# Kernel tuning notes

Measured on AMD Instinct MI355X. Metric: run time of the kernel, lower is better.

The kernel has to match this reference:

```python
import jax, jax.numpy as jnp
import numpy as np

B, N, F, K, FILT = 256, 256, 128, 4, 256  # batch mols, max_atom, Fin, Chebyshev order, nb_filter
EPS = float(np.spacing(np.float32(0)))    # matches np.spacing(0) in original degree normalization
D2_FLOOR = 1e-12                          # numerical floor for sqrt of pairwise sq-dist


def setup_inputs() -> dict:
    key = jax.random.key(0)
    ks = jax.random.split(key, 6)
    x = jax.random.normal(ks[0], (B, N, F), dtype=jnp.float32)
    lap_in = 0.1 * jax.random.normal(ks[1], (B, N, N), dtype=jnp.float32)  # input per-mol Laplacian
    n_atoms = jax.random.randint(ks[2], (B,), 64, N + 1, dtype=jnp.int32)  # ragged mol sizes
    r1 = float(np.sqrt(6.0 / (F + F)))
    M_L = jax.random.uniform(ks[3], (F, F), jnp.float32, -r1, r1)          # Mahalanobis metric
    r2 = float(np.sqrt(6.0 / (F * K + FILT)))
    weight = jax.random.uniform(ks[4], (F * K, FILT), jnp.float32, -r2, r2)
    bias = jnp.zeros((FILT,), jnp.float32)
    return {"x": x, "lap_in": lap_in, "n_atoms": n_atoms, "M_L": M_L, "weight": weight, "bias": bias}


def reference(x, lap_in, n_atoms, M_L, weight, bias):
    # mask[b,n] = 1 for real atoms, 0 for padding (replaces per-mol tf.slice + pad)
    mask = (jnp.arange(N)[None, :] < n_atoms[:, None]).astype(x.dtype)       # [B,N]
    x = x * mask[..., None]

    # ---- learned Laplacian: Mahalanobis RBF affinity + sym degree normalization ----
    xw = jnp.einsum('bnf,fg->bng', x, M_L)                                   # x @ M_L
    sq = jnp.sum(xw * xw, axis=-1)                                           # [B,N]
    d2 = sq[:, :, None] + sq[:, None, :] - 2.0 * jnp.einsum('bif,bjf->bij', xw, xw)
    eye = jnp.eye(N, dtype=x.dtype)
    off = mask[:, :, None] * mask[:, None, :] * (1.0 - eye)                  # valid off-diag pairs
    d2_safe = jnp.where(off > 0, jnp.maximum(d2, D2_FLOOR), 1.0)
    W = jnp.exp(-jnp.sqrt(d2_safe)) * off                                    # W[i,j]=exp(-dist), diag 0
    deg = jnp.sum(W, axis=1) + EPS                                           # W symmetric: axis0==axis1
    dinv = jnp.where(mask > 0, 1.0 / jnp.sqrt(deg), 0.0)                     # D^{-1/2} (0 on padding)
    # L = I - D^{-1/2} W D^{-1/2} (intended math of the original py_func)
    L_learn = eye[None] * mask[:, :, None] - dinv[:, :, None] * W * dinv[:, None, :]
    L = L_learn + lap_in * (mask[:, :, None] * mask[:, None, :])             # L + sliced input LL

    # ---- Chebyshev recurrence: x0=x, x1=Lx, xk = 2 L x_{k-1} - x_{k-2} ----
    x0 = x
    x1 = jnp.einsum('bij,bjf->bif', L, x0)
    xs = [x0, x1]
    for _ in range(2, K):
        x2 = 2.0 * jnp.einsum('bij,bjf->bif', L, x1) - x0
        xs.append(x2)
        x0, x1 = x1, x2
    # stack -> [B,N,F,K] then flatten (f,k) row-major, matching reshape([K,M,F])->transpose([1,2,0])->reshape([M,K*F])
    xc = jnp.stack(xs, axis=-1).reshape(B, N, F * K)

    out = jnp.einsum('bnd,do->bno', xc, weight) + bias                       # [B,N,FILT]
    out = jax.nn.relu(out * mask[..., None])                                 # pad-to-max_atom + relu
    return out, L_learn
```

## Files before the change

kernel.cpp:

```cpp
#include <hip/hip_runtime.h>
#include <math.h>

typedef __bf16 bf16;
typedef __bf16 bf16x8 __attribute__((ext_vector_type(8)));
typedef __bf16 bf16x4 __attribute__((ext_vector_type(4)));
typedef float f32x4 __attribute__((ext_vector_type(4)));

constexpr int cB = 256, cN = 256, cF = 128, cO = 256;
constexpr int BN = cB * cN;
constexpr float D2_FLOOR = 1e-12f;
constexpr float EPS_F = 1.401298464324817e-45f;

constexpr size_t OFF_XC  = 0;
constexpr size_t OFF_XW  = OFF_XC + (size_t)BN * 512 * 2;
constexpr size_t OFF_X0T = OFF_XW + (size_t)BN * 128 * 2;
constexpr size_t OFF_X1T = OFF_X0T + (size_t)cB * cF * cN * 2;
constexpr size_t OFF_X2T = OFF_X1T + (size_t)cB * cF * cN * 2;
constexpr size_t OFF_LB  = OFF_X2T + (size_t)cB * cF * cN * 2;
constexpr size_t OFF_WT  = OFF_LB + (size_t)cB * cN * cN * 2;
constexpr size_t OFF_MT  = OFF_WT + 512 * 256 * 2;
constexpr size_t OFF_SQ  = OFF_MT + 128 * 128 * 2;

__device__ __forceinline__ bf16x8 gfrag(const bf16* __restrict__ p, int ld,
                                        int lane, int k0) {
  return *(const bf16x8*)(p + (size_t)(lane & 15) * ld + k0 + 8 * (lane >> 4));
}

__device__ __forceinline__ f32x4 mfma(bf16x8 a, bf16x8 b, f32x4 c) {
  return __builtin_amdgcn_mfma_f32_16x16x32_bf16(a, b, c, 0, 0, 0);
}

__global__ __launch_bounds__(256) void k_prep(const float* __restrict__ x,
                                              const int* __restrict__ na_p,
                                              bf16* __restrict__ xc,
                                              bf16* __restrict__ x0T) {
  __shared__ __align__(16) bf16 T[64][132];
  int b = blockIdx.x >> 2, i0 = (blockIdx.x & 3) * 64;
  int tid = threadIdx.x;
  int na = na_p[b];
#pragma unroll
  for (int it = 0; it < 8; ++it) {
    int ir = it * 8 + (tid >> 5);
    int f0 = (tid & 31) * 4;
    int i = i0 + ir;
    float m = (i < na) ? 1.f : 0.f;
    float4 v = *(const float4*)(x + ((size_t)b * cN + i) * cF + f0);
    bf16x4 pk = {(bf16)(v.x * m), (bf16)(v.y * m), (bf16)(v.z * m), (bf16)(v.w * m)};
    *(bf16x4*)(xc + ((size_t)b * cN + i) * 512 + f0) = pk;
    *(bf16x4*)(&T[ir][f0]) = pk;
  }
  __syncthreads();
  int f = tid >> 1, half = tid & 1;
  bf16* od = x0T + ((size_t)b * cF + f) * cN + i0 + half * 32;
#pragma unroll
  for (int c = 0; c < 32; c += 4) {
    int ii = half * 32 + c;
    bf16x4 pk = {T[ii][f], T[ii + 1][f], T[ii + 2][f], T[ii + 3][f]};
    *(bf16x4*)(od + c) = pk;
  }
}

__global__ __launch_bounds__(256) void k_wt(const float* __restrict__ wgt,
                                            const float* __restrict__ ML,
                                            bf16* __restrict__ Wt,
                                            bf16* __restrict__ MT) {
  int id = blockIdx.x * 256 + threadIdx.x;
  if (id < 512 * 256) {
    int o = id >> 9, d = id & 511;
    int k = d >> 7, f = d & 127;
    Wt[id] = (bf16)wgt[(f * 4 + k) * 256 + o];
  } else {
    int id2 = id - 512 * 256;
    if (id2 < 128 * 128) {
      int g = id2 >> 7, f = id2 & 127;
      MT[id2] = (bf16)ML[f * 128 + g];
    }
  }
}

__global__ __launch_bounds__(256, 2) void k_xw2(const bf16* __restrict__ xc,
                                                const bf16* __restrict__ MT,
                                                bf16* __restrict__ xw,
                                                float* __restrict__ sq) {
  __shared__ float sqb[128];
  int tid = threadIdx.x, wid = tid >> 6, lane = tid & 63;
  int r0 = blockIdx.x * 128;
  const bf16* A = xc + (size_t)r0 * 512;
  const bf16* Bg = MT + (size_t)(wid * 32) * 128;
  f32x4 acc[8][2] = {};
#pragma unroll
  for (int ks = 0; ks < 4; ++ks) {
    int k0 = ks * 32;
    bf16x8 b0 = gfrag(Bg, 128, lane, k0);
    bf16x8 b1 = gfrag(Bg + 16 * 128, 128, lane, k0);
#pragma unroll
    for (int mf = 0; mf < 8; ++mf) {
      bf16x8 a = gfrag(A + (size_t)mf * 16 * 512, 512, lane, k0);
      acc[mf][0] = mfma(a, b0, acc[mf][0]);
      acc[mf][1] = mfma(a, b1, acc[mf][1]);
    }
  }
  if (tid < 128) sqb[tid] = 0.f;
  __syncthreads();
  int hi = lane >> 4, il = lane & 15;
#pragma unroll
  for (int mf = 0; mf < 8; ++mf) {
#pragma unroll
    for (int r = 0; r < 4; ++r) {
      int row = r0 + mf * 16 + 4 * hi + r;
      float s = 0.f;
#pragma unroll
      for (int nf = 0; nf < 2; ++nf) {
        bf16 v = (bf16)acc[mf][nf][r];
        xw[(size_t)row * cF + wid * 32 + nf * 16 + il] = v;
        float f = (float)v;
        s = fmaf(f, f, s);
      }
      s += __shfl_xor(s, 1); s += __shfl_xor(s, 2);
      s += __shfl_xor(s, 4); s += __shfl_xor(s, 8);
      if (il == 0) atomicAdd(&sqb[mf * 16 + 4 * hi + r], s);
    }
  }
  __syncthreads();
  if (tid < 128) sq[r0 + tid] = sqb[tid];
}

__global__ __launch_bounds__(512, 2) void k_gramL(const bf16* __restrict__ xw,
                                                  const float* __restrict__ sq,
                                                  const float* __restrict__ lap,
                                                  const int* __restrict__ na_p,
                                                  bf16* __restrict__ Lb,
                                                  float* __restrict__ llearn) {
  __shared__ float lsq[256];
  __shared__ float deg[256];
  __shared__ float dinv[256];
  int b = blockIdx.x, tid = threadIdx.x, wid = tid >> 6, lane = tid & 63;
  int wm = wid >> 2, wn = wid & 3;
  if (tid < 256) { lsq[tid] = sq[b * cN + tid]; deg[tid] = 0.f; }
  const bf16* X = xw + (size_t)b * cN * cF;
  const bf16* Ag = X + (size_t)(wm * 128) * cF;
  const bf16* Bg = X + (size_t)(wn * 64) * cF;
  f32x4 acc[8][4] = {};
#pragma unroll
  for (int ks = 0; ks < 4; ++ks) {
    int k0 = ks * 32;
    bf16x8 bb[4];
#pragma unroll
    for (int nf = 0; nf < 4; ++nf) bb[nf] = gfrag(Bg + (size_t)nf * 16 * cF, cF, lane, k0);
#pragma unroll
    for (int mf = 0; mf < 8; ++mf) {
      bf16x8 a = gfrag(Ag + (size_t)mf * 16 * cF, cF, lane, k0);
#pragma unroll
      for (int nf = 0; nf < 4; ++nf) acc[mf][nf] = mfma(a, bb[nf], acc[mf][nf]);
    }
  }
  __syncthreads();
  int na = na_p[b];
  int hi = lane >> 4, il = lane & 15;
#pragma unroll
  for (int mf = 0; mf < 8; ++mf) {
#pragma unroll
    for (int r = 0; r < 4; ++r) {
      int i = wm * 128 + mf * 16 + 4 * hi + r;
      float sqi = lsq[i];
      bool mi = i < na;
      float rs = 0.f;
#pragma unroll
      for (int nf = 0; nf < 4; ++nf) {
        int j = wn * 64 + nf * 16 + il;
        float w = 0.f;
        if (mi && j < na && i != j) {
          float d2 = fmaxf(sqi + lsq[j] - 2.f * acc[mf][nf][r], D2_FLOOR);
          w = __expf(-sqrtf(d2));
        }
        acc[mf][nf][r] = w;
        rs += w;
      }
      rs += __shfl_xor(rs, 1); rs += __shfl_xor(rs, 2);
      rs += __shfl_xor(rs, 4); rs += __shfl_xor(rs, 8);
      if (il == 0) atomicAdd(&deg[i], rs);
    }
  }
  __syncthreads();
  if (tid < 256) dinv[tid] = (tid < na) ? 1.f / sqrtf(deg[tid] + EPS_F) : 0.f;
  __syncthreads();
  const float* lapb = lap + (size_t)b * cN * cN;
  float* llb = llearn + (size_t)b * cN * cN;
  bf16* lbb = Lb + (size_t)b * cN * cN;
#pragma unroll
  for (int mf = 0; mf < 8; ++mf) {
#pragma unroll
    for (int r = 0; r < 4; ++r) {
      int i = wm * 128 + mf * 16 + 4 * hi + r;
      float di = dinv[i];
      float mi = (i < na) ? 1.f : 0.f;
#pragma unroll
      for (int nf = 0; nf < 4; ++nf) {
        int j = wn * 64 + nf * 16 + il;
        float v = -di * acc[mf][nf][r] * dinv[j];
        if (i == j && i < na) v += 1.f;
        size_t e = (size_t)i * cN + j;
        llb[e] = v;
        float mj = (j < na) ? 1.f : 0.f;
        lbb[e] = (bf16)(v + lapb[e] * mi * mj);
      }
    }
  }
}

template<bool BETA, bool WRITE_T>
__global__ __launch_bounds__(256, 2) void k_cheb2(const bf16* __restrict__ xT,
                                                  const bf16* __restrict__ Lb,
                                                  const bf16* __restrict__ xppT,
                                                  bf16* __restrict__ xoutT,
                                                  bf16* __restrict__ xc, int kcol) {
  int bx = blockIdx.x;
  int b = bx >> 1, i0 = (bx & 1) * 128;
  int tid = threadIdx.x, wid = tid >> 6, lane = tid & 63;
  const bf16* A = xT + (size_t)b * cF * cN;
  const bf16* Bg = Lb + (size_t)b * cN * cN + (size_t)(i0 + wid * 32) * cN;
  f32x4 acc[8][2] = {};
#pragma unroll
  for (int ks = 0; ks < 8; ++ks) {
    int k0 = ks * 32;
    bf16x8 b0 = gfrag(Bg, cN, lane, k0);
    bf16x8 b1 = gfrag(Bg + 16 * cN, cN, lane, k0);
#pragma unroll
    for (int mf = 0; mf < 8; ++mf) {
      bf16x8 a = gfrag(A + (size_t)mf * 16 * cN, cN, lane, k0);
      acc[mf][0] = mfma(a, b0, acc[mf][0]);
      acc[mf][1] = mfma(a, b1, acc[mf][1]);
    }
  }
  int hi = lane >> 4, il = lane & 15;
#pragma unroll
  for (int mf = 0; mf < 8; ++mf) {
#pragma unroll
    for (int nf = 0; nf < 2; ++nf) {
      int i = i0 + wid * 32 + nf * 16 + il;
#pragma unroll
      for (int r = 0; r < 4; ++r) {
        int f = mf * 16 + 4 * hi + r;
        float v = acc[mf][nf][r];
        if (BETA) v = 2.f * v - (float)xppT[(size_t)b * cF * cN + (size_t)f * cN + i];
        bf16 bv = (bf16)v;
        if (WRITE_T) xoutT[(size_t)b * cF * cN + (size_t)f * cN + i] = bv;
        xc[((size_t)b * cN + i) * 512 + kcol + f] = bv;
      }
    }
  }
}

__global__ __launch_bounds__(256, 2) void k_out2(const bf16* __restrict__ xc,
                                                 const bf16* __restrict__ Wt,
                                                 const float* __restrict__ bias,
                                                 const int* __restrict__ na_p,
                                                 float* __restrict__ out) {
  int tid = threadIdx.x, wid = tid >> 6, lane = tid & 63;
  int r0 = blockIdx.x * 128;
  const bf16* A = xc + (size_t)r0 * 512;
  const bf16* Bg = Wt + (size_t)(wid * 64) * 512;
  f32x4 acc[8][4] = {};
#pragma unroll 4
  for (int ks = 0; ks < 16; ++ks) {
    int k0 = ks * 32;
    bf16x8 bb[4];
#pragma unroll
    for (int nf = 0; nf < 4; ++nf) bb[nf] = gfrag(Bg + (size_t)nf * 16 * 512, 512, lane, k0);
#pragma unroll
    for (int mf = 0; mf < 8; ++mf) {
      bf16x8 a = gfrag(A + (size_t)mf * 16 * 512, 512, lane, k0);
#pragma unroll
      for (int nf = 0; nf < 4; ++nf) acc[mf][nf] = mfma(a, bb[nf], acc[mf][nf]);
    }
  }
  int na = na_p[r0 >> 8];
  int hi = lane >> 4, il = lane & 15;
#pragma unroll
  for (int nf = 0; nf < 4; ++nf) {
    int o = wid * 64 + nf * 16 + il;
    float bo = bias[o];
#pragma unroll
    for (int mf = 0; mf < 8; ++mf) {
#pragma unroll
      for (int r = 0; r < 4; ++r) {
        int row = r0 + mf * 16 + 4 * hi + r;
        float m = ((row & 255) < na) ? 1.f : 0.f;
        out[(size_t)row * cO + o] = fmaxf((acc[mf][nf][r] + bo) * m, 0.f);
      }
    }
  }
}

extern "C" void kernel_launch(void* const* d_in, const int* in_sizes, int n_in,
                              void* d_out, int out_size, void* d_ws, size_t ws_size,
                              hipStream_t stream) {
  const float* x    = (const float*)d_in[0];
  const float* lap  = (const float*)d_in[1];
  const int*   na   = (const int*)d_in[2];
  const float* M_L  = (const float*)d_in[3];
  const float* wgt  = (const float*)d_in[4];
  const float* bias = (const float*)d_in[5];

  float* out    = (float*)d_out;
  float* llearn = out + (size_t)BN * cO;

  char* ws = (char*)d_ws;
  bf16*  xc  = (bf16*)(ws + OFF_XC);
  bf16*  xw  = (bf16*)(ws + OFF_XW);
  bf16*  x0T = (bf16*)(ws + OFF_X0T);
  bf16*  x1T = (bf16*)(ws + OFF_X1T);
  bf16*  x2T = (bf16*)(ws + OFF_X2T);
  bf16*  Lb  = (bf16*)(ws + OFF_LB);
  bf16*  Wt  = (bf16*)(ws + OFF_WT);
  bf16*  MT  = (bf16*)(ws + OFF_MT);
  float* sqb = (float*)(ws + OFF_SQ);

  k_prep<<<dim3(1024), 256, 0, stream>>>(x, na, xc, x0T);
  k_wt<<<dim3(576), 256, 0, stream>>>(wgt, M_L, Wt, MT);
  k_xw2<<<dim3(512), 256, 0, stream>>>(xc, MT, xw, sqb);
  k_gramL<<<dim3(cB), 512, 0, stream>>>(xw, sqb, lap, na, Lb, llearn);
  k_cheb2<false, true><<<dim3(512), 256, 0, stream>>>(x0T, Lb, x0T, x1T, xc, 128);
  k_cheb2<true, true><<<dim3(512), 256, 0, stream>>>(x1T, Lb, x0T, x2T, xc, 256);
  k_cheb2<true, false><<<dim3(512), 256, 0, stream>>>(x2T, Lb, x1T, x2T, xc, 384);
  k_out2<<<dim3(512), 256, 0, stream>>>(xc, Wt, bias, na, out);
}
```

Measured before the change: 432.9 us.

## Fuse Chebyshev steps into one LDS-resident kernel and split gram/L assembly

```diff
diff --git a/kernel.cpp b/kernel.cpp
--- a/kernel.cpp
+++ b/kernel.cpp
@@ -14,12 +14,12 @@
 constexpr size_t OFF_XC  = 0;
 constexpr size_t OFF_XW  = OFF_XC + (size_t)BN * 512 * 2;
 constexpr size_t OFF_X0T = OFF_XW + (size_t)BN * 128 * 2;
-constexpr size_t OFF_X1T = OFF_X0T + (size_t)cB * cF * cN * 2;
-constexpr size_t OFF_X2T = OFF_X1T + (size_t)cB * cF * cN * 2;
-constexpr size_t OFF_LB  = OFF_X2T + (size_t)cB * cF * cN * 2;
-constexpr size_t OFF_WT  = OFF_LB + (size_t)cB * cN * cN * 2;
+constexpr size_t OFF_LB  = OFF_X0T + (size_t)cB * cF * cN * 2;
+constexpr size_t OFF_WB  = OFF_LB + (size_t)cB * cN * cN * 2;
+constexpr size_t OFF_WT  = OFF_WB + (size_t)cB * cN * cN * 2;
 constexpr size_t OFF_MT  = OFF_WT + 512 * 256 * 2;
 constexpr size_t OFF_SQ  = OFF_MT + 128 * 128 * 2;
+constexpr size_t OFF_DEG = OFF_SQ + (size_t)BN * 4;
 
 __device__ __forceinline__ bf16x8 gfrag(const bf16* __restrict__ p, int ld,
                                         int lane, int k0) {
@@ -28,6 +28,11 @@
 
 __device__ __forceinline__ f32x4 mfma(bf16x8 a, bf16x8 b, f32x4 c) {
   return __builtin_amdgcn_mfma_f32_16x16x32_bf16(a, b, c, 0, 0, 0);
+}
+
+__device__ __forceinline__ void gll16(const void* g, void* l) {
+  __builtin_amdgcn_global_load_lds((const __attribute__((address_space(1))) void*)g,
+                                   (__attribute__((address_space(3))) void*)l, 16, 0, 0);
 }
 
 __global__ __launch_bounds__(256) void k_prep(const float* __restrict__ x,
@@ -125,22 +130,23 @@
   if (tid < 128) sq[r0 + tid] = sqb[tid];
 }
 
-__global__ __launch_bounds__(512, 2) void k_gramL(const bf16* __restrict__ xw,
+__global__ __launch_bounds__(512, 2) void k_gram2(const bf16* __restrict__ xw,
                                                   const float* __restrict__ sq,
-                                                  const float* __restrict__ lap,
                                                   const int* __restrict__ na_p,
-                                                  bf16* __restrict__ Lb,
-                                                  float* __restrict__ llearn) {
+                                                  bf16* __restrict__ Wb16,
+                                                  float* __restrict__ deg) {
   __shared__ float lsq[256];
-  __shared__ float deg[256];
-  __shared__ float dinv[256];
-  int b = blockIdx.x, tid = threadIdx.x, wid = tid >> 6, lane = tid & 63;
+  __shared__ float degl[128];
+  int bx = blockIdx.x;
+  int b = bx >> 1, i0 = (bx & 1) * 128;
+  int tid = threadIdx.x, wid = tid >> 6, lane = tid & 63;
   int wm = wid >> 2, wn = wid & 3;
-  if (tid < 256) { lsq[tid] = sq[b * cN + tid]; deg[tid] = 0.f; }
+  if (tid < 256) lsq[tid] = sq[b * cN + tid];
+  if (tid < 128) degl[tid] = 0.f;
   const bf16* X = xw + (size_t)b * cN * cF;
-  const bf16* Ag = X + (size_t)(wm * 128) * cF;
+  const bf16* Ag = X + (size_t)(i0 + wm * 64) * cF;
   const bf16* Bg = X + (size_t)(wn * 64) * cF;
-  f32x4 acc[8][4] = {};
+  f32x4 acc[4][4] = {};
 #pragma unroll
   for (int ks = 0; ks < 4; ++ks) {
     int k0 = ks * 32;
@@ -148,7 +154,7 @@
 #pragma unroll
     for (int nf = 0; nf < 4; ++nf) bb[nf] = gfrag(Bg + (size_t)nf * 16 * cF, cF, lane, k0);
 #pragma unroll
-    for (int mf = 0; mf < 8; ++mf) {
+    for (int mf = 0; mf < 4; ++mf) {
       bf16x8 a = gfrag(Ag + (size_t)mf * 16 * cF, cF, lane, k0);
 #pragma unroll
       for (int nf = 0; nf < 4; ++nf) acc[mf][nf] = mfma(a, bb[nf], acc[mf][nf]);
@@ -158,10 +164,10 @@
   int na = na_p[b];
   int hi = lane >> 4, il = lane & 15;
 #pragma unroll
-  for (int mf = 0; mf < 8; ++mf) {
+  for (int mf = 0; mf < 4; ++mf) {
 #pragma unroll
     for (int r = 0; r < 4; ++r) {
-      int i = wm * 128 + mf * 16 + 4 * hi + r;
+      int i = i0 + wm * 64 + mf * 16 + 4 * hi + r;
       float sqi = lsq[i];
       bool mi = i < na;
       float rs = 0.f;
@@ -173,82 +179,119 @@
           float d2 = fmaxf(sqi + lsq[j] - 2.f * acc[mf][nf][r], D2_FLOOR);
           w = __expf(-sqrtf(d2));
         }
-        acc[mf][nf][r] = w;
+        Wb16[((size_t)b * cN + i) * cN + j] = (bf16)w;
         rs += w;
       }
       rs += __shfl_xor(rs, 1); rs += __shfl_xor(rs, 2);
       rs += __shfl_xor(rs, 4); rs += __shfl_xor(rs, 8);
-      if (il == 0) atomicAdd(&deg[i], rs);
-    }
-  }
-  __syncthreads();
-  if (tid < 256) dinv[tid] = (tid < na) ? 1.f / sqrtf(deg[tid] + EPS_F) : 0.f;
-  __syncthreads();
-  const float* lapb = lap + (size_t)b * cN * cN;
-  float* llb = llearn + (size_t)b * cN * cN;
-  bf16* lbb = Lb + (size_t)b * cN * cN;
-#pragma unroll
-  for (int mf = 0; mf < 8; ++mf) {
-#pragma unroll
-    for (int r = 0; r < 4; ++r) {
-      int i = wm * 128 + mf * 16 + 4 * hi + r;
-      float di = dinv[i];
-      float mi = (i < na) ? 1.f : 0.f;
-#pragma unroll
-      for (int nf = 0; nf < 4; ++nf) {
-        int j = wn * 64 + nf * 16 + il;
-        float v = -di * acc[mf][nf][r] * dinv[j];
-        if (i == j && i < na) v += 1.f;
-        size_t e = (size_t)i * cN + j;
-        llb[e] = v;
-        float mj = (j < na) ? 1.f : 0.f;
-        lbb[e] = (bf16)(v + lapb[e] * mi * mj);
-      }
-    }
-  }
-}
-
-template<bool BETA, bool WRITE_T>
-__global__ __launch_bounds__(256, 2) void k_cheb2(const bf16* __restrict__ xT,
-                                                  const bf16* __restrict__ Lb,
-                                                  const bf16* __restrict__ xppT,
-                                                  bf16* __restrict__ xoutT,
-                                                  bf16* __restrict__ xc, int kcol) {
-  int bx = blockIdx.x;
-  int b = bx >> 1, i0 = (bx & 1) * 128;
-  int tid = threadIdx.x, wid = tid >> 6, lane = tid & 63;
-  const bf16* A = xT + (size_t)b * cF * cN;
-  const bf16* Bg = Lb + (size_t)b * cN * cN + (size_t)(i0 + wid * 32) * cN;
-  f32x4 acc[8][2] = {};
+      if (il == 0) atomicAdd(&degl[i - i0], rs);
+    }
+  }
+  __syncthreads();
+  if (tid < 128) deg[b * cN + i0 + tid] = degl[tid];
+}
+
+__global__ __launch_bounds__(256) void k_Lassm(const bf16* __restrict__ Wb16,
+                                               const float* __restrict__ deg,
+                                               const float* __restrict__ lap,
+                                               const int* __restrict__ na_p,
+                                               bf16* __restrict__ Lb,
+                                               float* __restrict__ llearn) {
+  int tid = threadIdx.x;
+  size_t e = ((size_t)blockIdx.x * 256 + tid) * 4;
+  int b = (int)(e >> 16);
+  int na = na_p[b];
+  __shared__ float dinvl[256];
+  if (tid < 256) dinvl[tid] = (tid < na) ? 1.f / sqrtf(deg[b * cN + tid] + EPS_F) : 0.f;
+  __syncthreads();
+  int j = (int)(e & 255);
+  int i = (int)((e >> 8) & 255);
+  bf16x4 w4 = *(const bf16x4*)(Wb16 + e);
+  float4 lp = *(const float4*)(lap + e);
+  float di = dinvl[i];
+  float mi = (i < na) ? 1.f : 0.f;
+  float4 ll;
+  bf16x4 lo;
+#pragma unroll
+  for (int c = 0; c < 4; ++c) {
+    int jj = j + c;
+    float v = -di * (float)w4[c] * dinvl[jj];
+    if (i == jj && i < na) v += 1.f;
+    (&ll.x)[c] = v;
+    float mj = (jj < na) ? 1.f : 0.f;
+    lo[c] = (bf16)(v + (&lp.x)[c] * mi * mj);
+  }
+  *(float4*)(llearn + e) = ll;
+  *(bf16x4*)(Lb + e) = lo;
+}
+
+__device__ __forceinline__ void cheb_step(const bf16* __restrict__ Lm,
+                                          const char* Bsrc, const char* Ppp,
+                                          char* Odst, bf16* __restrict__ xcm,
+                                          int kcol, int wid, int lane, bool haspp,
+                                          bool wlds) {
+  int hi = lane >> 4, il = lane & 15;
+  int i0w = wid * 32;
+  f32x4 acc[2][8] = {};
 #pragma unroll
   for (int ks = 0; ks < 8; ++ks) {
     int k0 = ks * 32;
-    bf16x8 b0 = gfrag(Bg, cN, lane, k0);
-    bf16x8 b1 = gfrag(Bg + 16 * cN, cN, lane, k0);
-#pragma unroll
-    for (int mf = 0; mf < 8; ++mf) {
-      bf16x8 a = gfrag(A + (size_t)mf * 16 * cN, cN, lane, k0);
-      acc[mf][0] = mfma(a, b0, acc[mf][0]);
-      acc[mf][1] = mfma(a, b1, acc[mf][1]);
-    }
-  }
-  int hi = lane >> 4, il = lane & 15;
-#pragma unroll
-  for (int mf = 0; mf < 8; ++mf) {
-#pragma unroll
-    for (int nf = 0; nf < 2; ++nf) {
-      int i = i0 + wid * 32 + nf * 16 + il;
-#pragma unroll
-      for (int r = 0; r < 4; ++r) {
-        int f = mf * 16 + 4 * hi + r;
-        float v = acc[mf][nf][r];
-        if (BETA) v = 2.f * v - (float)xppT[(size_t)b * cF * cN + (size_t)f * cN + i];
-        bf16 bv = (bf16)v;
-        if (WRITE_T) xoutT[(size_t)b * cF * cN + (size_t)f * cN + i] = bv;
-        xc[((size_t)b * cN + i) * 512 + kcol + f] = bv;
+    bf16x8 a0 = gfrag(Lm + (size_t)i0w * cN, cN, lane, k0);
+    bf16x8 a1 = gfrag(Lm + (size_t)(i0w + 16) * cN, cN, lane, k0);
+#pragma unroll
+    for (int nf = 0; nf < 8; ++nf) {
+      int f = nf * 16 + il;
+      const char* p = Bsrc + f * 512 + ((64 * ks + 16 * hi) ^ ((il & 7) << 4));
+      bf16x8 bb = *(const bf16x8*)p;
+      acc[0][nf] = mfma(a0, bb, acc[0][nf]);
+      acc[1][nf] = mfma(a1, bb, acc[1][nf]);
+    }
+  }
+#pragma unroll
+  for (int mf = 0; mf < 2; ++mf) {
+    int ib = i0w + mf * 16 + 4 * hi;
+#pragma unroll
+    for (int nf = 0; nf < 8; ++nf) {
+      int f = nf * 16 + il;
+      int cb = (2 * ib) ^ ((il & 7) << 4);
+      bf16x4 o;
+      if (haspp) {
+        bf16x4 pp = *(const bf16x4*)(Ppp + f * 512 + cb);
+#pragma unroll
+        for (int r = 0; r < 4; ++r) o[r] = (bf16)(2.f * acc[mf][nf][r] - (float)pp[r]);
+      } else {
+#pragma unroll
+        for (int r = 0; r < 4; ++r) o[r] = (bf16)acc[mf][nf][r];
       }
-    }
-  }
+      if (wlds) *(bf16x4*)(Odst + f * 512 + cb) = o;
+#pragma unroll
+      for (int r = 0; r < 4; ++r)
+        xcm[(size_t)(ib + r) * 512 + kcol + f] = o[r];
+    }
+  }
+}
+
+__global__ __launch_bounds__(512, 1) void k_cheb_f(const bf16* __restrict__ x0T,
+                                                   const bf16* __restrict__ Lb,
+                                                   bf16* __restrict__ xc) {
+  __shared__ __align__(16) char XB[2][65536];
+  int b = blockIdx.x;
+  int tid = threadIdx.x, wid = tid >> 6, lane = tid & 63;
+  const bf16* Lm = Lb + (size_t)b * cN * cN;
+  bf16* xcm = xc + (size_t)b * cN * 512;
+  const char* src = (const char*)(x0T + (size_t)b * cF * cN);
+#pragma unroll
+  for (int it = 0; it < 8; ++it) {
+    int beta = it * 8192 + tid * 16;
+    int f = beta >> 9, c = beta & 511;
+    gll16(src + f * 512 + (c ^ ((f & 7) << 4)), XB[0] + beta);
+  }
+  __syncthreads();
+  cheb_step(Lm, XB[0], nullptr, XB[1], xcm, 128, wid, lane, false, true);
+  __syncthreads();
+  cheb_step(Lm, XB[1], XB[0], XB[0], xcm, 256, wid, lane, true, true);
+  __syncthreads();
+  cheb_step(Lm, XB[0], XB[1], nullptr, xcm, 384, wid, lane, true, false);
 }
 
 __global__ __launch_bounds__(256, 2) void k_out2(const bf16* __restrict__ xc,
@@ -309,19 +352,18 @@
   bf16*  xc  = (bf16*)(ws + OFF_XC);
   bf16*  xw  = (bf16*)(ws + OFF_XW);
   bf16*  x0T = (bf16*)(ws + OFF_X0T);
-  bf16*  x1T = (bf16*)(ws + OFF_X1T);
-  bf16*  x2T = (bf16*)(ws + OFF_X2T);
   bf16*  Lb  = (bf16*)(ws + OFF_LB);
+  bf16*  Wb  = (bf16*)(ws + OFF_WB);
   bf16*  Wt  = (bf16*)(ws + OFF_WT);
   bf16*  MT  = (bf16*)(ws + OFF_MT);
   float* sqb = (float*)(ws + OFF_SQ);
+  float* deg = (float*)(ws + OFF_DEG);
 
   k_prep<<<dim3(1024), 256, 0, stream>>>(x, na, xc, x0T);
   k_wt<<<dim3(576), 256, 0, stream>>>(wgt, M_L, Wt, MT);
   k_xw2<<<dim3(512), 256, 0, stream>>>(xc, MT, xw, sqb);
-  k_gramL<<<dim3(cB), 512, 0, stream>>>(xw, sqb, lap, na, Lb, llearn);
-  k_cheb2<false, true><<<dim3(512), 256, 0, stream>>>(x0T, Lb, x0T, x1T, xc, 128);
-  k_cheb2<true, true><<<dim3(512), 256, 0, stream>>>(x1T, Lb, x0T, x2T, xc, 256);
-  k_cheb2<true, false><<<dim3(512), 256, 0, stream>>>(x2T, Lb, x1T, x2T, xc, 384);
+  k_gram2<<<dim3(512), 512, 0, stream>>>(xw, sqb, na, Wb, deg);
+  k_Lassm<<<dim3(16384), 256, 0, stream>>>(Wb, deg, lap, na, Lb, llearn);
+  k_cheb_f<<<dim3(cB), 512, 0, stream>>>(x0T, Lb, xc);
   k_out2<<<dim3(512), 256, 0, stream>>>(xc, Wt, bias, na, out);
 }
```

Measured after the change: 380.6 us. -12.1%, faster.
